# Kernel optimization log

Hardware: AMD Instinct MI355X
Metric: run time of the kernel (lower is better)

Reference implementation:

```python
import jax, jax.numpy as jnp
import numpy as np

EPS = 1e-5

def layernorm(x, g, b):
    mu = jnp.mean(x, axis=-1, keepdims=True)
    var = jnp.mean(jnp.square(x - mu), axis=-1, keepdims=True)
    return (x - mu) * jax.lax.rsqrt(var + EPS) * g + b

def setup_inputs() -> dict:
    key = jax.random.key(0)
    ks = jax.random.split(key, 12)
    B, T, C, H = 4, 2048, 1024, 8
    Dh = C // H          # 128
    Dff = 4 * C          # 4096
    s = 0.02
    return {
        "x":     jax.random.normal(ks[0], (B, T, C), jnp.float32),
        "wq":    jax.random.normal(ks[1], (H, C, Dh), jnp.float32) * s,
        "wk":    jax.random.normal(ks[2], (H, C, Dh), jnp.float32) * s,
        "wv":    jax.random.normal(ks[3], (H, C, Dh), jnp.float32) * s,
        "w1":    jax.random.normal(ks[4], (C, Dff), jnp.float32) * s,
        "b1":    jnp.zeros((Dff,), jnp.float32),
        "w2":    jax.random.normal(ks[5], (Dff, C), jnp.float32) * s,
        "b2":    jnp.zeros((C,), jnp.float32),
        "ln1_g": jnp.ones((C,), jnp.float32),
        "ln1_b": jnp.zeros((C,), jnp.float32),
        "ln2_g": jnp.ones((C,), jnp.float32),
        "ln2_b": jnp.zeros((C,), jnp.float32),
    }

def reference(x, wq, wk, wv, w1, b1, w2, b2, ln1_g, ln1_b, ln2_g, ln2_b):
    B, T, C = x.shape
    H, _, Dh = wq.shape
    # --- multi-head self-attention (pre-LN) ---
    h = layernorm(x, ln1_g, ln1_b)
    q = jnp.einsum("btc,hcd->bhtd", h, wq)
    k = jnp.einsum("btc,hcd->bhtd", h, wk)
    v = jnp.einsum("btc,hcd->bhtd", h, wv)
    # NOTE: original multiplies by sqrt(head_size) (not divide) -- kept faithful
    scores = jnp.einsum("bhtd,bhsd->bhts", q, k) * (Dh ** 0.5)
    attn = jax.nn.softmax(scores, axis=-1)
    # dropout(p=0.2) treated as identity (eval mode)
    o = jnp.einsum("bhts,bhsd->bhtd", attn, v)
    # concat heads along last dim: head h fills contiguous slice
    o = o.transpose(0, 2, 1, 3).reshape(B, T, H * Dh)
    x = x + o  # no output projection in original module
    # --- feed-forward (pre-LN) ---
    h2 = layernorm(x, ln2_g, ln2_b)
    ff = jax.nn.relu(h2 @ w1 + b1) @ w2 + b2
    return x + ff
```

## Files before the change

kernel.cpp:

```cpp
#include <hip/hip_runtime.h>
#include <hip/hip_bf16.h>
#include <math.h>

#define B_   4
#define T_   2048
#define C_   1024
#define H_   8
#define DH   128
#define DFF  4096
#define M_   (B_*T_)

typedef __attribute__((ext_vector_type(8))) short bf16x8;
typedef __attribute__((ext_vector_type(4))) float f32x4;
typedef __attribute__((ext_vector_type(2))) unsigned int u32x2;

#define SC2 16.32223094f

__device__ __forceinline__ unsigned short f2bf(float x) {
  union { float f; unsigned u; } v; v.f = x;
  return (unsigned short)((v.u + 0x7fffu + ((v.u >> 16) & 1u)) >> 16);
}
__device__ __forceinline__ float bf2f(unsigned short h) {
  union { unsigned u; float f; } v; v.u = ((unsigned)h) << 16; return v.f;
}

__device__ __forceinline__ f32x4 mfma_bf16(bf16x8 a, bf16x8 b, f32x4 c) {
  return __builtin_amdgcn_mfma_f32_16x16x32_bf16(a, b, c, 0, 0, 0);
}

__device__ __forceinline__ void gll16(const void* g, void* l) {
  __builtin_amdgcn_global_load_lds((const __attribute__((address_space(1))) void*)g,
                                   (__attribute__((address_space(3))) void*)l,
                                   16, 0, 0);
}

__global__ __launch_bounds__(256) void ln_kernel(const float* __restrict__ in,
                                                 const float* __restrict__ g,
                                                 const float* __restrict__ bb,
                                                 unsigned short* __restrict__ h_hi,
                                                 unsigned short* __restrict__ h_lo) {
  __shared__ float red[8];
  const int row = blockIdx.x;
  const int tid = threadIdx.x;
  const float* p = in + (size_t)row * C_;
  const float4 xv = *(const float4*)(p + (tid << 2));
  float s  = xv.x + xv.y + xv.z + xv.w;
  float sq = xv.x*xv.x + xv.y*xv.y + xv.z*xv.z + xv.w*xv.w;
  #pragma unroll
  for (int off = 32; off > 0; off >>= 1) {
    s  += __shfl_xor(s, off);
    sq += __shfl_xor(sq, off);
  }
  if ((tid & 63) == 0) { red[(tid >> 6) * 2] = s; red[(tid >> 6) * 2 + 1] = sq; }
  __syncthreads();
  s  = red[0] + red[2] + red[4] + red[6];
  sq = red[1] + red[3] + red[5] + red[7];
  const float mu  = s * (1.0f / C_);
  const float var = sq * (1.0f / C_) - mu * mu;
  const float rs  = rsqrtf(var + 1e-5f);
  const float4 gv = *(const float4*)(g  + (tid << 2));
  const float4 bv = *(const float4*)(bb + (tid << 2));
  float ov[4];
  ov[0] = (xv.x - mu) * rs * gv.x + bv.x;
  ov[1] = (xv.y - mu) * rs * gv.y + bv.y;
  ov[2] = (xv.z - mu) * rs * gv.z + bv.z;
  ov[3] = (xv.w - mu) * rs * gv.w + bv.w;
  ushort4 hv, lv;
  unsigned short* hp = (unsigned short*)&hv;
  unsigned short* lp = (unsigned short*)&lv;
  #pragma unroll
  for (int j = 0; j < 4; ++j) {
    hp[j] = f2bf(ov[j]);
    lp[j] = f2bf(ov[j] - bf2f(hp[j]));
  }
  *(ushort4*)(h_hi + (size_t)row * C_ + (tid << 2)) = hv;
  *(ushort4*)(h_lo + (size_t)row * C_ + (tid << 2)) = lv;
}

__global__ __launch_bounds__(256) void cvt_t_kernel(const float* __restrict__ in,
                                                    unsigned short* __restrict__ out,
                                                    int R, int CC) {
  __shared__ float tile[32][33];
  const int r0 = blockIdx.y << 5, c0 = blockIdx.x << 5;
  const int tr = threadIdx.x >> 3, tc4 = (threadIdx.x & 7) << 2;
  const float4 vv = *(const float4*)(in + (size_t)(r0 + tr) * CC + c0 + tc4);
  tile[tr][tc4+0] = vv.x; tile[tr][tc4+1] = vv.y;
  tile[tr][tc4+2] = vv.z; tile[tr][tc4+3] = vv.w;
  __syncthreads();
  ushort4 o;
  o.x = f2bf(tile[tc4+0][tr]); o.y = f2bf(tile[tc4+1][tr]);
  o.z = f2bf(tile[tc4+2][tr]); o.w = f2bf(tile[tc4+3][tr]);
  *(ushort4*)(out + (size_t)(c0 + tr) * R + r0 + tc4) = o;
}

__global__ __launch_bounds__(256) void cvt_qkv_kernel(const float* __restrict__ wq,
                                                      const float* __restrict__ wk,
                                                      const float* __restrict__ wv,
                                                      unsigned short* __restrict__ wt_hi,
                                                      unsigned short* __restrict__ wt_lo) {
  const int z = blockIdx.z;
  const int which = z >> 3, head = z & 7;
  const float* in = (which == 0 ? wq : (which == 1 ? wk : wv)) + (size_t)head * C_ * DH;
  unsigned short* oh = wt_hi + (size_t)z * DH * C_;
  unsigned short* ol = wt_lo + (size_t)z * DH * C_;
  __shared__ float tile[32][33];
  const int r0 = blockIdx.y << 5, c0 = blockIdx.x << 5;
  const int tr = threadIdx.x >> 3, tc4 = (threadIdx.x & 7) << 2;
  const float4 vv = *(const float4*)(in + (size_t)(r0 + tr) * DH + c0 + tc4);
  tile[tr][tc4+0] = vv.x; tile[tr][tc4+1] = vv.y;
  tile[tr][tc4+2] = vv.z; tile[tr][tc4+3] = vv.w;
  __syncthreads();
  ushort4 hv, lv;
  unsigned short* hp = (unsigned short*)&hv;
  unsigned short* lp = (unsigned short*)&lv;
  #pragma unroll
  for (int j = 0; j < 4; ++j) {
    const float val = tile[tc4+j][tr];
    hp[j] = f2bf(val);
    lp[j] = f2bf(val - bf2f(hp[j]));
  }
  *(ushort4*)(oh + (size_t)(c0 + tr) * C_ + r0 + tc4) = hv;
  *(ushort4*)(ol + (size_t)(c0 + tr) * C_ + r0 + tc4) = lv;
}


__device__ __forceinline__ void gemm128_split3(
    const unsigned short* __restrict__ Ah, const unsigned short* __restrict__ Al,
    int lda,
    const unsigned short* __restrict__ Bh, const unsigned short* __restrict__ Bl,
    int ldb, int K, f32x4 (&acc)[4][4],
    unsigned short* AhS, unsigned short* AlS,
    unsigned short* BhS, unsigned short* BlS) {
  const int tid  = threadIdx.x;
  const int w    = tid >> 6;
  const int lane = tid & 63;
  const int l15  = lane & 15, quad = lane >> 4;
  const int srow = lane >> 2;
  const int skc  = ((lane & 3) << 3) ^ (((srow >> 1) & 3) << 3);
  const int wm = w & 1, wn = w >> 1;
  const int ro = ((quad ^ ((l15 >> 1) & 3)) << 3);

  for (int k0 = 0; k0 < K; k0 += 32) {
    __syncthreads();
    #pragma unroll
    for (int i = 0; i < 2; ++i) {
      const int seg  = w * 2 + i;
      const int r    = seg * 16 + srow;
      const int lofs = seg * 512 + lane * 8;
      gll16(Ah + (size_t)r * lda + k0 + skc, AhS + lofs);
      gll16(Bh + (size_t)r * ldb + k0 + skc, BhS + lofs);
      gll16(Al + (size_t)r * lda + k0 + skc, AlS + lofs);
      gll16(Bl + (size_t)r * ldb + k0 + skc, BlS + lofs);
    }
    __syncthreads();
    bf16x8 aH[4], bH[4], aL[4], bL[4];
    #pragma unroll
    for (int t = 0; t < 4; ++t) {
      aH[t] = *(const bf16x8*)&AhS[(wm * 64 + t * 16 + l15) * 32 + ro];
      bH[t] = *(const bf16x8*)&BhS[(wn * 64 + t * 16 + l15) * 32 + ro];
      aL[t] = *(const bf16x8*)&AlS[(wm * 64 + t * 16 + l15) * 32 + ro];
      bL[t] = *(const bf16x8*)&BlS[(wn * 64 + t * 16 + l15) * 32 + ro];
    }
    #pragma unroll
    for (int rt = 0; rt < 4; ++rt)
      #pragma unroll
      for (int ct = 0; ct < 4; ++ct) {
        acc[rt][ct] = mfma_bf16(aL[rt], bH[ct], acc[rt][ct]);
        acc[rt][ct] = mfma_bf16(aH[rt], bL[ct], acc[rt][ct]);
        acc[rt][ct] = mfma_bf16(aH[rt], bH[ct], acc[rt][ct]);
      }
  }
}

__device__ __forceinline__ void gemm128_db(
    const unsigned short* __restrict__ Ah, int lda,
    const unsigned short* __restrict__ Bh, int ldb, int K, f32x4 (&acc)[4][4],
    unsigned short (&AS0)[4096], unsigned short (&AS1)[4096],
    unsigned short (&BS0)[4096], unsigned short (&BS1)[4096]) {
  const int tid  = threadIdx.x;
  const int w    = tid >> 6;
  const int lane = tid & 63;
  const int l15  = lane & 15, quad = lane >> 4;
  const int srow = lane >> 2;
  const int skc  = ((lane & 3) << 3) ^ (((srow >> 1) & 3) << 3);
  const int wm = w & 1, wn = w >> 1;
  const int ro = ((quad ^ ((l15 >> 1) & 3)) << 3);
  const int Km = K - 1;

  auto STG = [&](int k0, unsigned short* A, unsigned short* B) {
    #pragma unroll
    for (int i = 0; i < 2; ++i) {
      const int seg  = w * 2 + i;
      const int r    = seg * 16 + srow;
      const int lofs = seg * 512 + lane * 8;
      gll16(Ah + (size_t)r * lda + k0 + skc, A + lofs);
      gll16(Bh + (size_t)r * ldb + k0 + skc, B + lofs);
    }
  };
  auto CMP = [&](const unsigned short* A, const unsigned short* B) {
    bf16x8 aH[4], bH[4];
    #pragma unroll
    for (int t = 0; t < 4; ++t) {
      aH[t] = *(const bf16x8*)&A[(wm * 64 + t * 16 + l15) * 32 + ro];
      bH[t] = *(const bf16x8*)&B[(wn * 64 + t * 16 + l15) * 32 + ro];
    }
    #pragma unroll
    for (int rt = 0; rt < 4; ++rt)
      #pragma unroll
      for (int ct = 0; ct < 4; ++ct)
        acc[rt][ct] = mfma_bf16(aH[rt], bH[ct], acc[rt][ct]);
  };

  STG(0, AS0, BS0);
  for (int k0 = 0; k0 < K; k0 += 64) {
    __syncthreads();
    STG((k0 + 32) & Km, AS1, BS1);
    CMP(AS0, BS0);
    __syncthreads();
    STG((k0 + 64) & Km, AS0, BS0);
    CMP(AS1, BS1);
  }
}

__global__ __launch_bounds__(256) void qkm_kernel(const unsigned short* __restrict__ h_hi,
                                                  const unsigned short* __restrict__ h_lo,
                                                  const unsigned short* __restrict__ wt_hi,
                                                  const unsigned short* __restrict__ wt_lo,
                                                  unsigned short* __restrict__ q_hi,
                                                  unsigned short* __restrict__ q_lo,
                                                  unsigned short* __restrict__ k_hi,
                                                  unsigned short* __restrict__ k_lo) {
  __shared__ __align__(16) unsigned short AhS[4096], AlS[4096];
  __shared__ __align__(16) unsigned short BhS[4096], BlS[4096];
  const int m0 = blockIdx.x << 7;
  const int z  = blockIdx.y;
  const int which = z >> 3, head = z & 7;
  f32x4 acc[4][4];
  #pragma unroll
  for (int i = 0; i < 4; ++i)
    #pragma unroll
    for (int j = 0; j < 4; ++j)
      #pragma unroll
      for (int r = 0; r < 4; ++r) acc[i][j][r] = 0.f;
  gemm128_split3(h_hi + (size_t)m0 * C_, h_lo + (size_t)m0 * C_, C_,
                 wt_hi + (size_t)z * DH * C_, wt_lo + (size_t)z * DH * C_, C_,
                 C_, acc, AhS, AlS, BhS, BlS);
  const int lane = threadIdx.x & 63, w = threadIdx.x >> 6;
  const int l15 = lane & 15, quad = lane >> 4;
  const int wm = w & 1, wn = w >> 1;
  const int bh = (m0 >> 11) * H_ + head;
  const int tbase = (m0 & (T_ - 1)) + wm * 64 + quad * 4;
  if (which == 0) {
    #pragma unroll
    for (int rt = 0; rt < 4; ++rt)
      #pragma unroll
      for (int ct = 0; ct < 4; ++ct) {
        const int d = wn * 64 + ct * 16 + l15;
        #pragma unroll
        for (int r = 0; r < 4; ++r) {
          const int t = tbase + rt * 16 + r;
          const float val = acc[rt][ct][r] * SC2;
          const unsigned short hb = f2bf(val);
          const size_t idx = ((size_t)bh * T_ + t) * DH + d;
          q_hi[idx] = hb;
          q_lo[idx] = f2bf(val - bf2f(hb));
        }
      }
  } else {
    #pragma unroll
    for (int rt = 0; rt < 4; ++rt)
      #pragma unroll
      for (int ct = 0; ct < 4; ++ct) {
        const int d = wn * 64 + ct * 16 + l15;
        #pragma unroll
        for (int r = 0; r < 4; ++r) {
          const int t = tbase + rt * 16 + r;
          const int tt = t & 31;
          const float val = acc[rt][ct][r];
          const unsigned short hb = f2bf(val);
          const size_t idx = (((size_t)bh * 64 + (t >> 5)) * 4 + (d >> 5)) * 1024
                           + (size_t)tt * 32 + ((d & 31) ^ (((tt >> 1) & 3) << 3));
          k_hi[idx] = hb;
          k_lo[idx] = f2bf(val - bf2f(hb));
        }
      }
  }
}

__global__ __launch_bounds__(256) void vm_kernel(const unsigned short* __restrict__ h_hi,
                                                 const unsigned short* __restrict__ wv_hi,
                                                 unsigned short* __restrict__ vimg) {
  __shared__ __align__(16) unsigned short AS0[4096], AS1[4096];
  __shared__ __align__(16) unsigned short BS0[4096], BS1[4096];
  const int m0 = blockIdx.x << 7;
  const int head = blockIdx.y;
  f32x4 acc[4][4];
  #pragma unroll
  for (int i = 0; i < 4; ++i)
    #pragma unroll
    for (int j = 0; j < 4; ++j)
      #pragma unroll
      for (int r = 0; r < 4; ++r) acc[i][j][r] = 0.f;
  gemm128_db(h_hi + (size_t)m0 * C_, C_,
             wv_hi + (size_t)(16 + head) * DH * C_, C_,
             C_, acc, AS0, AS1, BS0, BS1);
  const int lane = threadIdx.x & 63, w = threadIdx.x >> 6;
  const int l15 = lane & 15, quad = lane >> 4;
  const int wm = w & 1, wn = w >> 1;
  const int bh = (m0 >> 11) * H_ + head;
  #pragma unroll
  for (int rt = 0; rt < 4; ++rt)
    #pragma unroll
    for (int ct = 0; ct < 4; ++ct) {
      const int d  = wn * 64 + ct * 16 + l15;
      const int t0 = (m0 & (T_ - 1)) + wm * 64 + rt * 16 + quad * 4;
      const int key = (t0 & 31) ^ (((d >> 1) & 3) << 3);
      ushort4 pk;
      pk.x = f2bf(acc[rt][ct][0]); pk.y = f2bf(acc[rt][ct][1]);
      pk.z = f2bf(acc[rt][ct][2]); pk.w = f2bf(acc[rt][ct][3]);
      *(ushort4*)&vimg[(((size_t)bh * 64 + (t0 >> 5)) * 128 + d) * 32 + key] = pk;
    }
}

__global__ __launch_bounds__(256) void ff1_kernel(const unsigned short* __restrict__ h2,
                                                  const unsigned short* __restrict__ w1t,
                                                  const float* __restrict__ b1,
                                                  unsigned short* __restrict__ ff1) {
  __shared__ __align__(16) unsigned short AS0[4096], AS1[4096];
  __shared__ __align__(16) unsigned short BS0[4096], BS1[4096];
  const int n0 = blockIdx.x << 7;
  const int m0 = blockIdx.y << 7;
  f32x4 acc[4][4];
  #pragma unroll
  for (int i = 0; i < 4; ++i)
    #pragma unroll
    for (int j = 0; j < 4; ++j)
      #pragma unroll
      for (int r = 0; r < 4; ++r) acc[i][j][r] = 0.f;
  gemm128_db(h2 + (size_t)m0 * C_, C_,
             w1t + (size_t)n0 * C_, C_,
             C_, acc, AS0, AS1, BS0, BS1);
  const int lane = threadIdx.x & 63, w = threadIdx.x >> 6;
  const int l15 = lane & 15, quad = lane >> 4;
  const int wm = w & 1, wn = w >> 1;
  #pragma unroll
  for (int rt = 0; rt < 4; ++rt)
    #pragma unroll
    for (int ct = 0; ct < 4; ++ct) {
      const int n = n0 + wn * 64 + ct * 16 + l15;
      const float bias = b1[n];
      #pragma unroll
      for (int r = 0; r < 4; ++r) {
        const int m = m0 + wm * 64 + rt * 16 + quad * 4 + r;
        ff1[(size_t)m * DFF + n] = f2bf(fmaxf(acc[rt][ct][r] + bias, 0.f));
      }
    }
}

__global__ __launch_bounds__(256) void ff2_kernel(const unsigned short* __restrict__ ff1,
                                                  const unsigned short* __restrict__ w2t,
                                                  const float* __restrict__ b2,
                                                  const float* __restrict__ xo,
                                                  float* __restrict__ out) {
  __shared__ __align__(16) unsigned short AS0[4096], AS1[4096];
  __shared__ __align__(16) unsigned short BS0[4096], BS1[4096];
  const int n0 = blockIdx.x << 7;
  const int m0 = blockIdx.y << 7;
  f32x4 acc[4][4];
  #pragma unroll
  for (int i = 0; i < 4; ++i)
    #pragma unroll
    for (int j = 0; j < 4; ++j)
      #pragma unroll
      for (int r = 0; r < 4; ++r) acc[i][j][r] = 0.f;
  gemm128_db(ff1 + (size_t)m0 * DFF, DFF,
             w2t + (size_t)n0 * DFF, DFF,
             DFF, acc, AS0, AS1, BS0, BS1);
  const int lane = threadIdx.x & 63, w = threadIdx.x >> 6;
  const int l15 = lane & 15, quad = lane >> 4;
  const int wm = w & 1, wn = w >> 1;
  #pragma unroll
  for (int rt = 0; rt < 4; ++rt)
    #pragma unroll
    for (int ct = 0; ct < 4; ++ct) {
      const int n = n0 + wn * 64 + ct * 16 + l15;
      const float bias = b2[n];
      #pragma unroll
      for (int r = 0; r < 4; ++r) {
        const int m = m0 + wm * 64 + rt * 16 + quad * 4 + r;
        out[(size_t)m * C_ + n] = acc[rt][ct][r] + bias + xo[(size_t)m * C_ + n];
      }
    }
}

#define BQ 128

__global__ __launch_bounds__(512, 4) void attn_kernel(
    const unsigned short* __restrict__ q_hi, const unsigned short* __restrict__ q_lo,
    const unsigned short* __restrict__ k_hi, const unsigned short* __restrict__ k_lo,
    const unsigned short* __restrict__ vimg,
    const float* __restrict__ x, float* __restrict__ xo) {
  __shared__ __align__(16) unsigned short KhS[2][8192];
  __shared__ __align__(16) unsigned short KlS[8192];
  __shared__ __align__(16) unsigned short VtS[2][8192];

  const int bid   = blockIdx.x + (T_ / BQ) * blockIdx.y;
  const int chunk = bid >> 3;
  const int bh    = (bid & 7) * 4 + (chunk >> 4);
  const int qt0   = (chunk & 15) * BQ;

  const int tid  = threadIdx.x;
  const int w    = tid >> 6;
  const int lane = tid & 63;
  const int l15  = lane & 15;
  const int quad = lane >> 4;
  const int swz  = (l15 >> 1) & 3;
  const int sA   = ((quad & 1) << 5) + l15;
  const int sB   = sA + 16;
  const int bsel = (quad >> 1) & 1;

  bf16x8 Qh[4], Ql[4];
  {
    const int row = qt0 + w * 16 + l15;
    #pragma unroll
    for (int kc = 0; kc < 4; ++kc) {
      const size_t off = ((size_t)bh * T_ + row) * DH + kc * 32 + quad * 8;
      Qh[kc] = *(const bf16x8*)(q_hi + off);
      Ql[kc] = *(const bf16x8*)(q_lo + off);
    }
  }

  f32x4 O[8];
  #pragma unroll
  for (int n = 0; n < 8; ++n)
    #pragma unroll
    for (int r = 0; r < 4; ++r) O[n][r] = 0.f;
  float m_cur = -1e30f;
  float l_cur = 0.f;

  auto STAGE_K64 = [&](int jt) {
    const size_t tb = ((size_t)bh * 64 + (jt & 31) * 2) * 4096;
    unsigned short* KH = &KhS[jt & 1][0];
    const int o = tid * 8;
    gll16(k_hi + tb + o, KH + o);
    gll16(k_hi + tb + 4096 + o, KH + 4096 + o);
    gll16(k_lo + tb + o, KlS + o);
    gll16(k_lo + tb + 4096 + o, KlS + 4096 + o);
  };
  auto STAGE_V64 = [&](int jt) {
    const size_t tb = ((size_t)bh * 64 + jt * 2) * 4096;
    unsigned short* VT = &VtS[jt & 1][0];
    const int o = tid * 8;
    gll16(vimg + tb + o, VT + o);
    gll16(vimg + tb + 4096 + o, VT + 4096 + o);
  };

  bf16x8 bPp[2];

  STAGE_K64(0);

  for (int j = 0; j < T_ / 64; ++j) {
    __syncthreads();

    f32x4 S[4];
    #pragma unroll
    for (int ct = 0; ct < 4; ++ct)
      #pragma unroll
      for (int r = 0; r < 4; ++r) S[ct][r] = 0.f;
    {
      const unsigned short* KH = &KhS[j & 1][0];
      __builtin_amdgcn_s_setprio(1);
      #pragma unroll
      for (int sub = 0; sub < 2; ++sub)
        #pragma unroll
        for (int kc = 0; kc < 4; ++kc)
          #pragma unroll
          for (int c2 = 0; c2 < 2; ++c2) {
            const int o = sub * 4096 + kc * 1024 + (c2 * 16 + l15) * 32
                        + ((quad ^ swz) << 3);
            const bf16x8 kh = *(const bf16x8*)&KH[o];
            const bf16x8 kl = *(const bf16x8*)&KlS[o];
            f32x4& Sr = S[sub * 2 + c2];
            Sr = mfma_bf16(kl, Qh[kc], Sr);
            Sr = mfma_bf16(kh, Ql[kc], Sr);
            Sr = mfma_bf16(kh, Qh[kc], Sr);
          }
      __builtin_amdgcn_s_setprio(0);
    }

    __syncthreads();
    STAGE_K64(j + 1);
    STAGE_V64(j);

    if (j > 0) {
      const unsigned short* VT = &VtS[(j - 1) & 1][0];
      __builtin_amdgcn_s_setprio(1);
      #pragma unroll
      for (int g = 0; g < 2; ++g)
        #pragma unroll
        for (int n = 0; n < 8; ++n) {
          const bf16x8 av =
              *(const bf16x8*)&VT[g * 4096 + (n * 16 + l15) * 32 + ((quad ^ swz) << 3)];
          O[n] = mfma_bf16(av, bPp[g], O[n]);
        }
      __builtin_amdgcn_s_setprio(0);
    }

    float mx = -1e30f;
    #pragma unroll
    for (int ct = 0; ct < 4; ++ct)
      mx = fmaxf(mx, fmaxf(fmaxf(S[ct][0], S[ct][1]), fmaxf(S[ct][2], S[ct][3])));
    mx = fmaxf(mx, __shfl_xor(mx, 16));
    mx = fmaxf(mx, __shfl_xor(mx, 32));

    if (__any(mx > m_cur + 8.f)) {
      const float mn = fmaxf(m_cur, mx);
      const float al = exp2f(m_cur - mn);
      m_cur = mn;
      l_cur *= al;
      #pragma unroll
      for (int n = 0; n < 8; ++n)
        #pragma unroll
        for (int r = 0; r < 4; ++r) O[n][r] *= al;
    }

    unsigned pu[8];
    float rs = 0.f;
    #pragma unroll
    for (int ct = 0; ct < 4; ++ct) {
      const float p0 = exp2f(S[ct][0] - m_cur);
      const float p1 = exp2f(S[ct][1] - m_cur);
      const float p2 = exp2f(S[ct][2] - m_cur);
      const float p3 = exp2f(S[ct][3] - m_cur);
      rs += (p0 + p1) + (p2 + p3);
      pu[ct * 2 + 0] = (__float_as_uint(p1) & 0xffff0000u) | (__float_as_uint(p0) >> 16);
      pu[ct * 2 + 1] = (__float_as_uint(p3) & 0xffff0000u) | (__float_as_uint(p2) >> 16);
    }
    rs += __shfl_xor(rs, 16);
    rs += __shfl_xor(rs, 32);
    l_cur += rs;

    #pragma unroll
    for (int g = 0; g < 2; ++g) {
      const unsigned xA0 = (unsigned)__shfl((int)pu[4 * g + 0], sA);
      const unsigned yA0 = (unsigned)__shfl((int)pu[4 * g + 2], sA);
      const unsigned xA1 = (unsigned)__shfl((int)pu[4 * g + 1], sA);
      const unsigned yA1 = (unsigned)__shfl((int)pu[4 * g + 3], sA);
      const unsigned xB0 = (unsigned)__shfl((int)pu[4 * g + 0], sB);
      const unsigned yB0 = (unsigned)__shfl((int)pu[4 * g + 2], sB);
      const unsigned xB1 = (unsigned)__shfl((int)pu[4 * g + 1], sB);
      const unsigned yB1 = (unsigned)__shfl((int)pu[4 * g + 3], sB);
      union { unsigned u[4]; bf16x8 v; } cv;
      cv.u[0] = bsel ? yA0 : xA0;
      cv.u[1] = bsel ? yA1 : xA1;
      cv.u[2] = bsel ? yB0 : xB0;
      cv.u[3] = bsel ? yB1 : xB1;
      bPp[g] = cv.v;
    }
  }

  __syncthreads();
  {
    const unsigned short* VT = &VtS[(T_ / 64 - 1) & 1][0];
    #pragma unroll
    for (int g = 0; g < 2; ++g)
      #pragma unroll
      for (int n = 0; n < 8; ++n) {
        const bf16x8 av =
            *(const bf16x8*)&VT[g * 4096 + (n * 16 + l15) * 32 + ((quad ^ swz) << 3)];
        O[n] = mfma_bf16(av, bPp[g], O[n]);
      }
  }

  const int b = bh >> 3, hh = bh & 7;
  const float inv_l = 1.0f / l_cur;
  const int t = qt0 + w * 16 + l15;
  const size_t xrow = ((size_t)(b * T_ + t)) * C_ + (size_t)hh * DH;
  #pragma unroll
  for (int n = 0; n < 8; ++n) {
    const int d = n * 16 + quad * 4;
    const float4 xv = *(const float4*)(x + xrow + d);
    float4 ov;
    ov.x = xv.x + O[n][0] * inv_l;
    ov.y = xv.y + O[n][1] * inv_l;
    ov.z = xv.z + O[n][2] * inv_l;
    ov.w = xv.w + O[n][3] * inv_l;
    *(float4*)(xo + xrow + d) = ov;
  }
}

extern "C" void kernel_launch(void* const* d_in, const int* in_sizes, int n_in,
                              void* d_out, int out_size, void* d_ws, size_t ws_size,
                              hipStream_t stream) {
  (void)in_sizes; (void)n_in; (void)out_size; (void)ws_size;
  const float* x     = (const float*)d_in[0];
  const float* wq    = (const float*)d_in[1];
  const float* wk    = (const float*)d_in[2];
  const float* wv    = (const float*)d_in[3];
  const float* w1    = (const float*)d_in[4];
  const float* b1    = (const float*)d_in[5];
  const float* w2    = (const float*)d_in[6];
  const float* b2    = (const float*)d_in[7];
  const float* ln1_g = (const float*)d_in[8];
  const float* ln1_b = (const float*)d_in[9];
  const float* ln2_g = (const float*)d_in[10];
  const float* ln2_b = (const float*)d_in[11];
  float* out = (float*)d_out;

  char* W = (char*)d_ws;
  float* xo = (float*)(W);
  unsigned short* q_hi  = (unsigned short*)(W + (32u  << 20));
  unsigned short* q_lo  = (unsigned short*)(W + (48u  << 20));
  unsigned short* k_hi  = (unsigned short*)(W + (64u  << 20));
  unsigned short* k_lo  = (unsigned short*)(W + (80u  << 20));
  unsigned short* vimg  = (unsigned short*)(W + (96u  << 20));
  unsigned short* ff1   = (unsigned short*)(W + (32u  << 20));
  unsigned short* h_hi  = (unsigned short*)(W + (112u << 20));
  unsigned short* h_lo  = (unsigned short*)(W + (128u << 20));
  unsigned short* w1t   = (unsigned short*)(W + (144u << 20));
  unsigned short* w2t   = (unsigned short*)(W + (152u << 20));
  unsigned short* wt_hi = (unsigned short*)(W + (160u << 20));
  unsigned short* wt_lo = (unsigned short*)(W + (166u << 20));

  cvt_t_kernel<<<dim3(DFF / 32, C_ / 32), 256, 0, stream>>>(w1, w1t, C_, DFF);
  cvt_t_kernel<<<dim3(C_ / 32, DFF / 32), 256, 0, stream>>>(w2, w2t, DFF, C_);
  cvt_qkv_kernel<<<dim3(DH / 32, C_ / 32, 24), 256, 0, stream>>>(wq, wk, wv, wt_hi, wt_lo);
  ln_kernel<<<M_, 256, 0, stream>>>(x, ln1_g, ln1_b, h_hi, h_lo);
  qkm_kernel<<<dim3(M_ / 128, 16), 256, 0, stream>>>(h_hi, h_lo, wt_hi, wt_lo,
                                                     q_hi, q_lo, k_hi, k_lo);
  vm_kernel<<<dim3(M_ / 128, H_), 256, 0, stream>>>(h_hi, wt_hi, vimg);
  attn_kernel<<<dim3(T_ / BQ, B_ * H_), 512, 0, stream>>>(q_hi, q_lo, k_hi, k_lo,
                                                          vimg, x, xo);
  ln_kernel<<<M_, 256, 0, stream>>>(xo, ln2_g, ln2_b, h_hi, h_lo);
  ff1_kernel<<<dim3(DFF / 128, M_ / 128), 256, 0, stream>>>(h_hi, w1t, b1, ff1);
  ff2_kernel<<<dim3(C_ / 128, M_ / 128), 256, 0, stream>>>(ff1, w2t, b2, xo, out);
}
```

Baseline: 651.2 us.

## Prefetch K and V together one tile ahead with a single barrier per iteration

The attention loop now double-buffers the low K tile as well, and stages the next tile's K-hi, K-lo and V in one call right after a single barrier. Each iteration then runs QK, softmax and PV on the current tile. This replaces the old scheme, which used two barriers per iteration and deferred PV by one iteration. The goal is to cut barrier overhead and give global loads a full iteration to land. In exchange, LDS use rises to about 96KB per block and launch bounds drop to 2, which likely lowers occupancy. The overlap that came from deferring PV behind the next tile's QK is also lost.

```diff
diff --git a/kernel.cpp b/kernel.cpp
--- a/kernel.cpp
+++ b/kernel.cpp
@@ -395,13 +395,13 @@
 
 #define BQ 128
 
-__global__ __launch_bounds__(512, 4) void attn_kernel(
+__global__ __launch_bounds__(512, 2) void attn_kernel(
     const unsigned short* __restrict__ q_hi, const unsigned short* __restrict__ q_lo,
     const unsigned short* __restrict__ k_hi, const unsigned short* __restrict__ k_lo,
     const unsigned short* __restrict__ vimg,
     const float* __restrict__ x, float* __restrict__ xo) {
   __shared__ __align__(16) unsigned short KhS[2][8192];
-  __shared__ __align__(16) unsigned short KlS[8192];
+  __shared__ __align__(16) unsigned short KlS[2][8192];
   __shared__ __align__(16) unsigned short VtS[2][8192];
 
   const int bid   = blockIdx.x + (T_ / BQ) * blockIdx.y;
@@ -438,29 +438,25 @@
   float m_cur = -1e30f;
   float l_cur = 0.f;
 
-  auto STAGE_K64 = [&](int jt) {
+  auto STAGE64 = [&](int jt) {
     const size_t tb = ((size_t)bh * 64 + (jt & 31) * 2) * 4096;
     unsigned short* KH = &KhS[jt & 1][0];
+    unsigned short* KL = &KlS[jt & 1][0];
+    unsigned short* VT = &VtS[jt & 1][0];
     const int o = tid * 8;
     gll16(k_hi + tb + o, KH + o);
     gll16(k_hi + tb + 4096 + o, KH + 4096 + o);
-    gll16(k_lo + tb + o, KlS + o);
-    gll16(k_lo + tb + 4096 + o, KlS + 4096 + o);
-  };
-  auto STAGE_V64 = [&](int jt) {
-    const size_t tb = ((size_t)bh * 64 + jt * 2) * 4096;
-    unsigned short* VT = &VtS[jt & 1][0];
-    const int o = tid * 8;
+    gll16(k_lo + tb + o, KL + o);
+    gll16(k_lo + tb + 4096 + o, KL + 4096 + o);
     gll16(vimg + tb + o, VT + o);
     gll16(vimg + tb + 4096 + o, VT + 4096 + o);
   };
 
-  bf16x8 bPp[2];
-
-  STAGE_K64(0);
+  STAGE64(0);
 
   for (int j = 0; j < T_ / 64; ++j) {
     __syncthreads();
+    STAGE64(j + 1);
 
     f32x4 S[4];
     #pragma unroll
@@ -469,6 +465,7 @@
       for (int r = 0; r < 4; ++r) S[ct][r] = 0.f;
     {
       const unsigned short* KH = &KhS[j & 1][0];
+      const unsigned short* KL = &KlS[j & 1][0];
       __builtin_amdgcn_s_setprio(1);
       #pragma unroll
       for (int sub = 0; sub < 2; ++sub)
@@ -479,30 +476,12 @@
             const int o = sub * 4096 + kc * 1024 + (c2 * 16 + l15) * 32
                         + ((quad ^ swz) << 3);
             const bf16x8 kh = *(const bf16x8*)&KH[o];
-            const bf16x8 kl = *(const bf16x8*)&KlS[o];
+            const bf16x8 kl = *(const bf16x8*)&KL[o];
             f32x4& Sr = S[sub * 2 + c2];
             Sr = mfma_bf16(kl, Qh[kc], Sr);
             Sr = mfma_bf16(kh, Ql[kc], Sr);
             Sr = mfma_bf16(kh, Qh[kc], Sr);
           }
-      __builtin_amdgcn_s_setprio(0);
-    }
-
-    __syncthreads();
-    STAGE_K64(j + 1);
-    STAGE_V64(j);
-
-    if (j > 0) {
-      const unsigned short* VT = &VtS[(j - 1) & 1][0];
-      __builtin_amdgcn_s_setprio(1);
-      #pragma unroll
-      for (int g = 0; g < 2; ++g)
-        #pragma unroll
-        for (int n = 0; n < 8; ++n) {
-          const bf16x8 av =
-              *(const bf16x8*)&VT[g * 4096 + (n * 16 + l15) * 32 + ((quad ^ swz) << 3)];
-          O[n] = mfma_bf16(av, bPp[g], O[n]);
-        }
       __builtin_amdgcn_s_setprio(0);
     }
 
@@ -540,6 +519,7 @@
     rs += __shfl_xor(rs, 32);
     l_cur += rs;
 
+    bf16x8 bP[2];
     #pragma unroll
     for (int g = 0; g < 2; ++g) {
       const unsigned xA0 = (unsigned)__shfl((int)pu[4 * g + 0], sA);
@@ -555,21 +535,22 @@
       cv.u[1] = bsel ? yA1 : xA1;
       cv.u[2] = bsel ? yB0 : xB0;
       cv.u[3] = bsel ? yB1 : xB1;
-      bPp[g] = cv.v;
-    }
-  }
-
-  __syncthreads();
-  {
-    const unsigned short* VT = &VtS[(T_ / 64 - 1) & 1][0];
-    #pragma unroll
-    for (int g = 0; g < 2; ++g)
-      #pragma unroll
-      for (int n = 0; n < 8; ++n) {
-        const bf16x8 av =
-            *(const bf16x8*)&VT[g * 4096 + (n * 16 + l15) * 32 + ((quad ^ swz) << 3)];
-        O[n] = mfma_bf16(av, bPp[g], O[n]);
-      }
+      bP[g] = cv.v;
+    }
+
+    {
+      const unsigned short* VT = &VtS[j & 1][0];
+      __builtin_amdgcn_s_setprio(1);
+      #pragma unroll
+      for (int g = 0; g < 2; ++g)
+        #pragma unroll
+        for (int n = 0; n < 8; ++n) {
+          const bf16x8 av =
+              *(const bf16x8*)&VT[g * 4096 + (n * 16 + l15) * 32 + ((quad ^ swz) << 3)];
+          O[n] = mfma_bf16(av, bP[g], O[n]);
+        }
+      __builtin_amdgcn_s_setprio(0);
+    }
   }
 
   const int b = bh >> 3, hh = bh & 7;
```

Measured after the change: 656.9 us. No clear change (+0.9%).
